# Optimization experiments

Measured on AMD Instinct MI355X. Metric: run time of the kernel, lower is better.

The kernel has to match this reference:

```python
import jax, jax.numpy as jnp
import numpy as np

B, P, NTIME, NLATENT, NSPATIAL = 4, 2, 16, 32, 2048


def sqrt_act(x):
    # signed square root: sign(x) * sqrt(|x|) (odd, monotone activation used in ERA5_PredRNN)
    return jnp.sign(x) * jnp.sqrt(jnp.abs(x))


def setup_inputs() -> dict:
    key = jax.random.key(0)
    ks = jax.random.split(key, 10)
    T, C, X = NTIME, NLATENT, NSPATIAL
    # xavier-uniform bounds (torch fan_in = T*C, fan_out = T*C for (t,T,c); T,T for 2D)
    s3 = (6.0 / (T * C + T * C)) ** 0.5
    s2 = (6.0 / (T + T)) ** 0.5
    x = jax.random.normal(ks[0], (B, P, T, C, X), jnp.float32)
    K0 = jax.random.uniform(ks[1], (T, T, C), jnp.float32, -s3, s3)
    Q0 = jax.random.uniform(ks[2], (T, T, C), jnp.float32, -s3, s3)
    V0 = jax.random.uniform(ks[3], (T, T, C), jnp.float32, -s3, s3)
    K1 = jax.random.uniform(ks[4], (T, T), jnp.float32, -s2, s2)
    Q1 = jax.random.uniform(ks[5], (T, T), jnp.float32, -s2, s2)
    V1 = jax.random.uniform(ks[6], (T, T), jnp.float32, -s2, s2)

    def ortho3(kk):
        # mimics nn.init.orthogonal_ on (T,T,T): rows (flattened to T x T*T) are orthonormal
        m = jax.random.normal(kk, (T * T, T), jnp.float32)
        q, _ = jnp.linalg.qr(m)  # (T*T, T), orthonormal columns
        return q.T.reshape(T, T, T)

    enc = ortho3(ks[7])
    dec = ortho3(ks[8])
    a = jnp.ones((T, X), jnp.float32)
    w = jnp.ones((T, X), jnp.float32) / (X * T)
    return dict(x=x, K0=K0, Q0=Q0, V0=V0, K1=K1, Q1=Q1, V1=V1,
                enc=enc, dec=dec, a=a, w=w)


def reference(x, K0, Q0, V0, K1, Q1, V1, enc, dec, a, w):
    # --- layer 0: per-latent-channel time mixing (tTc) ---
    k = jnp.einsum('tTc,bpTcx->bptcx', K0, x)
    q0 = jnp.einsum('tTc,bpTcx->bptcx', Q0, x)
    v = jnp.einsum('tTc,bpTcx->bptcx', V0, x)
    h = sqrt_act(jnp.einsum('bptcx,bpTcx,etT->bpecx', k, v, enc))
    # --- layer 1: shared time mixing (tT) ---
    k = jnp.einsum('tT,bpTcx->bptcx', K1, h)
    q1 = jnp.einsum('tT,bpTcx->bptcx', Q1, h)
    v = jnp.einsum('tT,bpTcx->bptcx', V1, h)
    h = sqrt_act(jnp.einsum('bptcx,bpTcx,etT->bpecx', k, v, enc))
    # estp: 'tx,bptcx->bptcx' (elementwise over t,x)
    b = a[None, None, :, None, :] * h
    # decoder mixing in reverse layer order (estb)
    b = jnp.einsum('bptcx,bpecx,etT->bpTcx', q1, b, dec)
    b = jnp.einsum('bptcx,bpecx,etT->bpTcx', q0, b, dec)
    # estc: 'tx,bptcx->bpc'
    y = jnp.einsum('tx,bptcx->bpc', w, b)
    return y[:, :, None, :]  # [B, p, 1, c]
```

## Files before the change

kernel.cpp:

```cpp
#include <hip/hip_runtime.h>
#include <math.h>

#define NB 4
#define NP 2
#define NT 16
#define NC 32
#define NX 2048
#define HS 20


typedef _Float16 f16x8 __attribute__((ext_vector_type(8)));
typedef float f32x16 __attribute__((ext_vector_type(16)));

__device__ __forceinline__ unsigned short f16hi_bits(float v) {
    _Float16 h = (_Float16)v;
    return __builtin_bit_cast(unsigned short, h);
}
__device__ __forceinline__ unsigned short f16lo_bits(float v) {
    _Float16 h = (_Float16)v;
    _Float16 l = (_Float16)(v - (float)h);
    return __builtin_bit_cast(unsigned short, l);
}
__device__ __forceinline__ f16x8 frag_cast(uint4 u) {
    return __builtin_bit_cast(f16x8, u);
}
__device__ __forceinline__ float sqrt_act(float v) {
    return copysignf(sqrtf(fabsf(v)), v);
}
__device__ __forceinline__ f32x16 zero16() {
    f32x16 z;
#pragma unroll
    for (int i = 0; i < 16; ++i) z[i] = 0.f;
    return z;
}

__device__ void g_compute(const float* __restrict__ K,
                          const float* __restrict__ V,
                          const float* __restrict__ enc,
                          int cstride, int c, int e, int tid,
                          float* sK, float* sV, float* sE, float* sW,
                          float* outG) {
    {
        const int t = tid >> 4, A = tid & 15;
        sK[tid] = K[(t * 16 + A) * cstride + c];
        sV[tid] = V[(t * 16 + A) * cstride + c];
        sE[tid] = enc[(e * 16 + t) * 16 + A];
    }
    __syncthreads();
    {
        const int t = tid >> 4, Bi = tid & 15;
        float acc = 0.f;
#pragma unroll
        for (int T = 0; T < 16; ++T) acc += sE[t * 16 + T] * sV[T * 16 + Bi];
        sW[tid] = acc;
    }
    __syncthreads();
    {
        const int A = tid >> 4, Bi = tid & 15;
        float acc = 0.f;
#pragma unroll
        for (int t = 0; t < 16; ++t) acc += sK[t * 16 + A] * sW[t * 16 + Bi];
        outG[tid] = acc;
    }
    __syncthreads();
}

__device__ void emit_half(const float* sG, uint4* __restrict__ dstPair,
                          int half, int tid) {
    if (tid < 64) {
        const int row = tid & 15, g = (tid >> 4) & 1, part = tid >> 5;
        unsigned dw[4];
#pragma unroll
        for (int d = 0; d < 4; ++d) {
            const float v0 = sG[row * 16 + g * 8 + 2 * d];
            const float v1 = sG[row * 16 + g * 8 + 2 * d + 1];
            const unsigned short s0 = part ? f16lo_bits(v0) : f16hi_bits(v0);
            const unsigned short s1 = part ? f16lo_bits(v1) : f16hi_bits(v1);
            dw[d] = (unsigned)s0 | ((unsigned)s1 << 16);
        }
        dstPair[part * 64 + g * 32 + 16 * half + row] =
            make_uint4(dw[0], dw[1], dw[2], dw[3]);
    }
}

__global__ __launch_bounds__(256) void precompute_all(
    const float* __restrict__ K0, const float* __restrict__ V0,
    const float* __restrict__ K1, const float* __restrict__ V1,
    const float* __restrict__ Q0, const float* __restrict__ Q1,
    const float* __restrict__ enc, const float* __restrict__ dec,
    uint4* __restrict__ AF0, uint4* __restrict__ AFG1,
    uint4* __restrict__ AFM1, uint4* __restrict__ AFM2,
    float* __restrict__ out) {
    __shared__ float sK[256], sV[256], sE[256], sW[256], sG[256];
    const int b = blockIdx.x, tid = threadIdx.x;
    if (b < 512) {
        const int c = b >> 4, e = b & 15;
        g_compute(K0, V0, enc, NC, c, e, tid, sK, sV, sE, sW, sG);
        emit_half(sG, AF0 + (c * 8 + (e >> 1)) * 128, e & 1, tid);
    } else if (b < 528) {
        const int e = b - 512;
        g_compute(K1, V1, enc, 1, 0, e, tid, sK, sV, sE, sW, sG);
        emit_half(sG, AFG1 + (e >> 1) * 128, e & 1, tid);
    } else if (b < 536) {
        const int m = b - 528;
        if (tid < 128) {
            const int part = tid >> 6, lane = tid & 63;
            const int row32 = lane & 31, g = lane >> 5;
            const int e = 2 * m + (row32 >> 4), E = row32 & 15;
            unsigned dw[4];
#pragma unroll
            for (int d = 0; d < 4; ++d) {
                unsigned short s01[2];
#pragma unroll
                for (int hh = 0; hh < 2; ++hh) {
                    const int T = g * 8 + 2 * d + hh;
                    float acc = 0.f;
#pragma unroll
                    for (int t = 0; t < 16; ++t)
                        acc += Q1[t * 16 + T] * dec[(e * 16 + t) * 16 + E];
                    s01[hh] = part ? f16lo_bits(acc) : f16hi_bits(acc);
                }
                dw[d] = (unsigned)s01[0] | ((unsigned)s01[1] << 16);
            }
            AFM1[m * 128 + part * 64 + lane] = make_uint4(dw[0], dw[1], dw[2], dw[3]);
        }
    } else if (b < 792) {
        const int idx = b - 536;
        const int c = idx >> 3, m = idx & 7;
        if (tid < 128) {
            const int part = tid >> 6, lane = tid & 63;
            const int row32 = lane & 31, g = lane >> 5;
            const int T = 2 * m + (row32 >> 4), A = row32 & 15;
            unsigned dw[4];
#pragma unroll
            for (int d = 0; d < 4; ++d) {
                unsigned short s01[2];
#pragma unroll
                for (int hh = 0; hh < 2; ++hh) {
                    const int E = g * 8 + 2 * d + hh;
                    float acc = 0.f;
#pragma unroll
                    for (int t = 0; t < 16; ++t)
                        acc += Q0[(t * 16 + A) * NC + c] * dec[(E * 16 + t) * 16 + T];
                    s01[hh] = part ? f16lo_bits(acc) : f16hi_bits(acc);
                }
                dw[d] = (unsigned)s01[0] | ((unsigned)s01[1] << 16);
            }
            AFM2[(c * 8 + m) * 128 + part * 64 + lane] =
                make_uint4(dw[0], dw[1], dw[2], dw[3]);
        }
    } else {
        if (tid < 128) AFM2[256 * 128 + tid] = make_uint4(0u, 0u, 0u, 0u);
        out[tid] = 0.f;
    }
}

__global__ __launch_bounds__(256) void site_kernel(
    const float* __restrict__ x,
    const float* __restrict__ a,
    const float* __restrict__ w,
    const uint4* __restrict__ AF0,
    const uint4* __restrict__ AFG1,
    const uint4* __restrict__ AFM1,
    const uint4* __restrict__ AFM2,
    float* __restrict__ out) {
    __shared__ float hlds[4][32 * HS];
    __shared__ float red[4];

    const int tid = threadIdx.x;
    const int lane = tid & 63, wid = tid >> 6;
    const int col = lane & 31, g = lane >> 5;
    const int bid = blockIdx.x;
    const int xg = bid & 15;
    const int c  = (bid >> 4) & 31;
    const int bp = bid >> 9;
    const int xA = xg * 128 + wid * 32 + col;
    const float* xb = x + (bp * NT * NC + c) * NX;
    float* hl = hlds[wid];

    f16x8 Xh, Xl;
    float XC[8];
#pragma unroll
    for (int j = 0; j < 8; ++j) {
        const float v = xb[(g * 8 + j) * NC * NX + xA];
        const _Float16 h = (_Float16)v;
        Xh[j] = h; Xl[j] = (_Float16)(v - (float)h);
    }
#pragma unroll
    for (int r = 0; r < 8; ++r) {
        const int A = (r & 3) + 8 * (r >> 2) + 4 * g;
        XC[r] = xb[A * NC * NX + xA];
    }

    {
        const uint4* p0 = AF0 + (c * 8) * 128;
#pragma unroll 1
        for (int m = 0; m < 8; ++m) {
            const f16x8 Ah = frag_cast(p0[lane]);
            const f16x8 Al = frag_cast(p0[64 + lane]);
            p0 += 128;
            f32x16 C = zero16();
            C = __builtin_amdgcn_mfma_f32_32x32x16_f16(Ah, Xh, C, 0, 0, 0);
            C = __builtin_amdgcn_mfma_f32_32x32x16_f16(Ah, Xl, C, 0, 0, 0);
            C = __builtin_amdgcn_mfma_f32_32x32x16_f16(Al, Xh, C, 0, 0, 0);
            float se = 0.f, so = 0.f;
#pragma unroll
            for (int r = 0; r < 8; ++r) {
                se += XC[r] * C[r];
                so += XC[r] * C[r + 8];
            }
            se += __shfl_xor(se, 32);
            so += __shfl_xor(so, 32);
            hl[col * HS + 2 * m]     = sqrt_act(se);
            hl[col * HS + 2 * m + 1] = sqrt_act(so);
        }
    }

    f16x8 hH, hL;
    float hC[8];
#pragma unroll
    for (int j = 0; j < 8; ++j) {
        const float v = hl[col * HS + g * 8 + j];
        const _Float16 h = (_Float16)v;
        hH[j] = h; hL[j] = (_Float16)(v - (float)h);
    }
#pragma unroll
    for (int r = 0; r < 8; ++r)
        hC[r] = hl[col * HS + (r & 3) + 8 * (r >> 2) + 4 * g];

    float b2[8];
#pragma unroll
    for (int r = 0; r < 8; ++r) b2[r] = 0.f;
    {
        const uint4* pG = AFG1;
        const uint4* pM = AFM1;
        const float* pa = a + xA;
#pragma unroll 1
        for (int m = 0; m < 8; ++m) {
            const f16x8 GH = frag_cast(pG[lane]);
            const f16x8 GL = frag_cast(pG[64 + lane]);
            const f16x8 MH = frag_cast(pM[lane]);
            const f16x8 ML = frag_cast(pM[64 + lane]);
            pG += 128; pM += 128;
            const float ae = pa[0], ao = pa[NX];
            pa += 2 * NX;
            f32x16 C = zero16();
            C = __builtin_amdgcn_mfma_f32_32x32x16_f16(GH, hH, C, 0, 0, 0);
            C = __builtin_amdgcn_mfma_f32_32x32x16_f16(GH, hL, C, 0, 0, 0);
            C = __builtin_amdgcn_mfma_f32_32x32x16_f16(GL, hH, C, 0, 0, 0);
            float se = 0.f, so = 0.f;
#pragma unroll
            for (int r = 0; r < 8; ++r) {
                se += hC[r] * C[r];
                so += hC[r] * C[r + 8];
            }
            se += __shfl_xor(se, 32);
            so += __shfl_xor(so, 32);
            const float pe = ae * sqrt_act(se);
            const float po = ao * sqrt_act(so);
            f32x16 U = zero16();
            U = __builtin_amdgcn_mfma_f32_32x32x16_f16(MH, hH, U, 0, 0, 0);
            U = __builtin_amdgcn_mfma_f32_32x32x16_f16(MH, hL, U, 0, 0, 0);
            U = __builtin_amdgcn_mfma_f32_32x32x16_f16(ML, hH, U, 0, 0, 0);
#pragma unroll
            for (int r = 0; r < 8; ++r)
                b2[r] += pe * U[r] + po * U[r + 8];
        }
    }

#pragma unroll
    for (int r = 0; r < 4; ++r) {
        hl[col * HS + r + 4 * g]     = b2[r];
        hl[col * HS + 8 + r + 4 * g] = b2[r + 4];
    }
    f16x8 bH, bL;
#pragma unroll
    for (int j = 0; j < 8; ++j) {
        const float v = hl[col * HS + g * 8 + j];
        const _Float16 h = (_Float16)v;
        bH[j] = h; bL[j] = (_Float16)(v - (float)h);
    }

    float ya = 0.f;
    {
        const uint4* p2 = AFM2 + (c * 8) * 128;
        const float* pw = w + xA;
#pragma unroll 1
        for (int m = 0; m < 8; ++m) {
            const f16x8 MH = frag_cast(p2[lane]);
            const f16x8 ML = frag_cast(p2[64 + lane]);
            p2 += 128;
            const float we = pw[0], wo = pw[NX];
            pw += 2 * NX;
            f32x16 Z = zero16();
            Z = __builtin_amdgcn_mfma_f32_32x32x16_f16(MH, bH, Z, 0, 0, 0);
            Z = __builtin_amdgcn_mfma_f32_32x32x16_f16(MH, bL, Z, 0, 0, 0);
            Z = __builtin_amdgcn_mfma_f32_32x32x16_f16(ML, bH, Z, 0, 0, 0);
            float se = 0.f, so = 0.f;
#pragma unroll
            for (int r = 0; r < 8; ++r) {
                se += XC[r] * Z[r];
                so += XC[r] * Z[r + 8];
            }
            ya += we * se + wo * so;
        }
    }

    float y = ya + __shfl_xor(ya, 32);
    y += __shfl_xor(y, 1); y += __shfl_xor(y, 2);
    y += __shfl_xor(y, 4); y += __shfl_xor(y, 8); y += __shfl_xor(y, 16);
    if (lane == 0) red[wid] = y;
    __syncthreads();
    if (tid == 0) {
        atomicAdd(&out[bp * NC + c], red[0] + red[1] + red[2] + red[3]);
    }
}

extern "C" void kernel_launch(void* const* d_in, const int* in_sizes, int n_in,
                              void* d_out, int out_size, void* d_ws, size_t ws_size,
                              hipStream_t stream) {
    const float* x   = (const float*)d_in[0];
    const float* K0  = (const float*)d_in[1];
    const float* Q0  = (const float*)d_in[2];
    const float* V0  = (const float*)d_in[3];
    const float* K1  = (const float*)d_in[4];
    const float* Q1  = (const float*)d_in[5];
    const float* V1  = (const float*)d_in[6];
    const float* enc = (const float*)d_in[7];
    const float* dec = (const float*)d_in[8];
    const float* a   = (const float*)d_in[9];
    const float* w   = (const float*)d_in[10];
    float* out = (float*)d_out;

    uint4* AF0  = (uint4*)d_ws;
    uint4* AFG1 = AF0  + 256 * 128;
    uint4* AFM1 = AFG1 + 8 * 128;
    uint4* AFM2 = AFM1 + 8 * 128;

    precompute_all<<<793, 256, 0, stream>>>(K0, V0, K1, V1, Q0, Q1,
                                            enc, dec, AF0, AFG1, AFM1, AFM2,
                                            out);

    const int nblocks = NB * NP * NC * (NX / 128);
    site_kernel<<<nblocks, 256, 0, stream>>>(x, a, w, AF0, AFG1, AFM1, AFM2, out);
}
```

Baseline: 168.4 us.

## Keep site intermediates in registers, unroll MFMA loops, stage dec in LDS

The site kernel stops staging h and b2 through per-wave LDS buffers. It keeps them in registers and uses a cross-half lane shuffle to rebuild the MFMA B fragments. The three MFMA loops are fully unrolled with offset-indexed loads, launch bounds request four blocks per CU, and sqrt uses the AMDGCN sqrt builtin. The precompute blocks now stage dec and Q into shared memory, and the zero-padding store for AFM2 is removed. Full unrolling raises register pressure, and dropping the padding write could matter if anything reads that region.

```diff
diff --git a/kernel.cpp b/kernel.cpp
--- a/kernel.cpp
+++ b/kernel.cpp
@@ -6,7 +6,6 @@
 #define NT 16
 #define NC 32
 #define NX 2048
-#define HS 20
 
 
 typedef _Float16 f16x8 __attribute__((ext_vector_type(8)));
@@ -25,7 +24,8 @@
     return __builtin_bit_cast(f16x8, u);
 }
 __device__ __forceinline__ float sqrt_act(float v) {
-    return copysignf(sqrtf(fabsf(v)), v);
+    const float s = __builtin_amdgcn_sqrtf(__builtin_fabsf(v));
+    return copysignf(s, v);
 }
 __device__ __forceinline__ f32x16 zero16() {
     f32x16 z;
@@ -92,6 +92,7 @@
     uint4* __restrict__ AFM1, uint4* __restrict__ AFM2,
     float* __restrict__ out) {
     __shared__ float sK[256], sV[256], sE[256], sW[256], sG[256];
+    __shared__ float sDec[4096], sQ[256];
     const int b = blockIdx.x, tid = threadIdx.x;
     if (b < 512) {
         const int c = b >> 4, e = b & 15;
@@ -103,6 +104,10 @@
         emit_half(sG, AFG1 + (e >> 1) * 128, e & 1, tid);
     } else if (b < 536) {
         const int m = b - 528;
+#pragma unroll
+        for (int i = tid; i < 4096; i += 256) sDec[i] = dec[i];
+        sQ[tid] = Q1[tid];
+        __syncthreads();
         if (tid < 128) {
             const int part = tid >> 6, lane = tid & 63;
             const int row32 = lane & 31, g = lane >> 5;
@@ -117,7 +122,7 @@
                     float acc = 0.f;
 #pragma unroll
                     for (int t = 0; t < 16; ++t)
-                        acc += Q1[t * 16 + T] * dec[(e * 16 + t) * 16 + E];
+                        acc += sQ[t * 16 + T] * sDec[(e * 16 + t) * 16 + E];
                     s01[hh] = part ? f16lo_bits(acc) : f16hi_bits(acc);
                 }
                 dw[d] = (unsigned)s01[0] | ((unsigned)s01[1] << 16);
@@ -127,6 +132,10 @@
     } else if (b < 792) {
         const int idx = b - 536;
         const int c = idx >> 3, m = idx & 7;
+#pragma unroll
+        for (int i = tid; i < 4096; i += 256) sDec[i] = dec[i];
+        sQ[tid] = Q0[tid * NC + c];
+        __syncthreads();
         if (tid < 128) {
             const int part = tid >> 6, lane = tid & 63;
             const int row32 = lane & 31, g = lane >> 5;
@@ -141,7 +150,7 @@
                     float acc = 0.f;
 #pragma unroll
                     for (int t = 0; t < 16; ++t)
-                        acc += Q0[(t * 16 + A) * NC + c] * dec[(E * 16 + t) * 16 + T];
+                        acc += sQ[t * 16 + A] * sDec[(E * 16 + t) * 16 + T];
                     s01[hh] = part ? f16lo_bits(acc) : f16hi_bits(acc);
                 }
                 dw[d] = (unsigned)s01[0] | ((unsigned)s01[1] << 16);
@@ -150,12 +159,11 @@
                 make_uint4(dw[0], dw[1], dw[2], dw[3]);
         }
     } else {
-        if (tid < 128) AFM2[256 * 128 + tid] = make_uint4(0u, 0u, 0u, 0u);
         out[tid] = 0.f;
     }
 }
 
-__global__ __launch_bounds__(256) void site_kernel(
+__global__ __launch_bounds__(256, 4) void site_kernel(
     const float* __restrict__ x,
     const float* __restrict__ a,
     const float* __restrict__ w,
@@ -164,27 +172,26 @@
     const uint4* __restrict__ AFM1,
     const uint4* __restrict__ AFM2,
     float* __restrict__ out) {
-    __shared__ float hlds[4][32 * HS];
     __shared__ float red[4];
 
     const int tid = threadIdx.x;
     const int lane = tid & 63, wid = tid >> 6;
     const int col = lane & 31, g = lane >> 5;
+    const bool g0 = (g == 0);
     const int bid = blockIdx.x;
     const int xg = bid & 15;
     const int c  = (bid >> 4) & 31;
     const int bp = bid >> 9;
     const int xA = xg * 128 + wid * 32 + col;
     const float* xb = x + (bp * NT * NC + c) * NX;
-    float* hl = hlds[wid];
 
     f16x8 Xh, Xl;
     float XC[8];
 #pragma unroll
     for (int j = 0; j < 8; ++j) {
         const float v = xb[(g * 8 + j) * NC * NX + xA];
-        const _Float16 h = (_Float16)v;
-        Xh[j] = h; Xl[j] = (_Float16)(v - (float)h);
+        const _Float16 hv = (_Float16)v;
+        Xh[j] = hv; Xl[j] = (_Float16)(v - (float)hv);
     }
 #pragma unroll
     for (int r = 0; r < 8; ++r) {
@@ -192,15 +199,16 @@
         XC[r] = xb[A * NC * NX + xA];
     }
 
-    {
-        const uint4* p0 = AF0 + (c * 8) * 128;
-#pragma unroll 1
+    const f32x16 Z0 = zero16();
+
+    float h[16];
+    {
+        const uint4* p0 = AF0 + (c * 8) * 128 + lane;
+#pragma unroll
         for (int m = 0; m < 8; ++m) {
-            const f16x8 Ah = frag_cast(p0[lane]);
-            const f16x8 Al = frag_cast(p0[64 + lane]);
-            p0 += 128;
-            f32x16 C = zero16();
-            C = __builtin_amdgcn_mfma_f32_32x32x16_f16(Ah, Xh, C, 0, 0, 0);
+            const f16x8 Ah = frag_cast(p0[m * 128]);
+            const f16x8 Al = frag_cast(p0[m * 128 + 64]);
+            f32x16 C = __builtin_amdgcn_mfma_f32_32x32x16_f16(Ah, Xh, Z0, 0, 0, 0);
             C = __builtin_amdgcn_mfma_f32_32x32x16_f16(Ah, Xl, C, 0, 0, 0);
             C = __builtin_amdgcn_mfma_f32_32x32x16_f16(Al, Xh, C, 0, 0, 0);
             float se = 0.f, so = 0.f;
@@ -211,8 +219,8 @@
             }
             se += __shfl_xor(se, 32);
             so += __shfl_xor(so, 32);
-            hl[col * HS + 2 * m]     = sqrt_act(se);
-            hl[col * HS + 2 * m + 1] = sqrt_act(so);
+            h[2 * m]     = sqrt_act(se);
+            h[2 * m + 1] = sqrt_act(so);
         }
     }
 
@@ -220,32 +228,32 @@
     float hC[8];
 #pragma unroll
     for (int j = 0; j < 8; ++j) {
-        const float v = hl[col * HS + g * 8 + j];
-        const _Float16 h = (_Float16)v;
-        hH[j] = h; hL[j] = (_Float16)(v - (float)h);
-    }
-#pragma unroll
-    for (int r = 0; r < 8; ++r)
-        hC[r] = hl[col * HS + (r & 3) + 8 * (r >> 2) + 4 * g];
+        const float v = g0 ? h[j] : h[j + 8];
+        const _Float16 hv = (_Float16)v;
+        hH[j] = hv; hL[j] = (_Float16)(v - (float)hv);
+    }
+#pragma unroll
+    for (int r = 0; r < 8; ++r) {
+        const int base = (r & 3) + 8 * (r >> 2);
+        hC[r] = g0 ? h[base] : h[base + 4];
+    }
 
     float b2[8];
 #pragma unroll
     for (int r = 0; r < 8; ++r) b2[r] = 0.f;
     {
-        const uint4* pG = AFG1;
-        const uint4* pM = AFM1;
+        const uint4* pG = AFG1 + lane;
+        const uint4* pM = AFM1 + lane;
         const float* pa = a + xA;
-#pragma unroll 1
+#pragma unroll
         for (int m = 0; m < 8; ++m) {
-            const f16x8 GH = frag_cast(pG[lane]);
-            const f16x8 GL = frag_cast(pG[64 + lane]);
-            const f16x8 MH = frag_cast(pM[lane]);
-            const f16x8 ML = frag_cast(pM[64 + lane]);
-            pG += 128; pM += 128;
-            const float ae = pa[0], ao = pa[NX];
-            pa += 2 * NX;
-            f32x16 C = zero16();
-            C = __builtin_amdgcn_mfma_f32_32x32x16_f16(GH, hH, C, 0, 0, 0);
+            const f16x8 GH = frag_cast(pG[m * 128]);
+            const f16x8 GL = frag_cast(pG[m * 128 + 64]);
+            const f16x8 MH = frag_cast(pM[m * 128]);
+            const f16x8 ML = frag_cast(pM[m * 128 + 64]);
+            const float ae = pa[(2 * m) * NX];
+            const float ao = pa[(2 * m + 1) * NX];
+            f32x16 C = __builtin_amdgcn_mfma_f32_32x32x16_f16(GH, hH, Z0, 0, 0, 0);
             C = __builtin_amdgcn_mfma_f32_32x32x16_f16(GH, hL, C, 0, 0, 0);
             C = __builtin_amdgcn_mfma_f32_32x32x16_f16(GL, hH, C, 0, 0, 0);
             float se = 0.f, so = 0.f;
@@ -258,8 +266,7 @@
             so += __shfl_xor(so, 32);
             const float pe = ae * sqrt_act(se);
             const float po = ao * sqrt_act(so);
-            f32x16 U = zero16();
-            U = __builtin_amdgcn_mfma_f32_32x32x16_f16(MH, hH, U, 0, 0, 0);
+            f32x16 U = __builtin_amdgcn_mfma_f32_32x32x16_f16(MH, hH, Z0, 0, 0, 0);
             U = __builtin_amdgcn_mfma_f32_32x32x16_f16(MH, hL, U, 0, 0, 0);
             U = __builtin_amdgcn_mfma_f32_32x32x16_f16(ML, hH, U, 0, 0, 0);
 #pragma unroll
@@ -268,32 +275,30 @@
         }
     }
 
+    f16x8 bH, bL;
 #pragma unroll
     for (int r = 0; r < 4; ++r) {
-        hl[col * HS + r + 4 * g]     = b2[r];
-        hl[col * HS + 8 + r + 4 * g] = b2[r + 4];
-    }
-    f16x8 bH, bL;
-#pragma unroll
-    for (int j = 0; j < 8; ++j) {
-        const float v = hl[col * HS + g * 8 + j];
-        const _Float16 h = (_Float16)v;
-        bH[j] = h; bL[j] = (_Float16)(v - (float)h);
+        const float snd = g0 ? b2[r + 4] : b2[r];
+        const float rcv = __shfl_xor(snd, 32);
+        const float v0 = g0 ? b2[r] : rcv;
+        const float v1 = g0 ? rcv : b2[r + 4];
+        _Float16 hv = (_Float16)v0;
+        bH[r] = hv;     bL[r]     = (_Float16)(v0 - (float)hv);
+        hv = (_Float16)v1;
+        bH[r + 4] = hv; bL[r + 4] = (_Float16)(v1 - (float)hv);
     }
 
     float ya = 0.f;
     {
-        const uint4* p2 = AFM2 + (c * 8) * 128;
+        const uint4* p2 = AFM2 + (c * 8) * 128 + lane;
         const float* pw = w + xA;
-#pragma unroll 1
+#pragma unroll
         for (int m = 0; m < 8; ++m) {
-            const f16x8 MH = frag_cast(p2[lane]);
-            const f16x8 ML = frag_cast(p2[64 + lane]);
-            p2 += 128;
-            const float we = pw[0], wo = pw[NX];
-            pw += 2 * NX;
-            f32x16 Z = zero16();
-            Z = __builtin_amdgcn_mfma_f32_32x32x16_f16(MH, bH, Z, 0, 0, 0);
+            const f16x8 MH = frag_cast(p2[m * 128]);
+            const f16x8 ML = frag_cast(p2[m * 128 + 64]);
+            const float we = pw[(2 * m) * NX];
+            const float wo = pw[(2 * m + 1) * NX];
+            f32x16 Z = __builtin_amdgcn_mfma_f32_32x32x16_f16(MH, bH, Z0, 0, 0, 0);
             Z = __builtin_amdgcn_mfma_f32_32x32x16_f16(MH, bL, Z, 0, 0, 0);
             Z = __builtin_amdgcn_mfma_f32_32x32x16_f16(ML, bH, Z, 0, 0, 0);
             float se = 0.f, so = 0.f;
```

Measured after the change: 174.3 us. 1.04x slower.
